# Kernel optimization log

Hardware: AMD Instinct MI355X
Metric: run time of the kernel (lower is better)

The kernel has to match this reference:

```python
import jax, jax.numpy as jnp
import numpy as np

B, S, D, H = 32, 8192, 128, 128


def setup_inputs() -> dict:
    key = jax.random.key(0)
    ks = jax.random.split(key, 8)
    x = jax.random.normal(ks[0], (B, D), dtype=jnp.float32)
    context = jax.random.normal(ks[1], (B, S, D), dtype=jnp.float32)
    mask = jax.random.bernoulli(ks[2], 0.3, (B, S))
    mask = mask.at[:, 0].set(False)
    W_in = jax.random.normal(ks[3], (H, D), dtype=jnp.float32) / np.sqrt(D)
    b_in = jax.random.normal(ks[4], (H,), dtype=jnp.float32) * 0.01
    # torch Conv1d(D, H, 1) weight is [H, D, 1]; squeeze kernel dim -> [H, D]
    W_ctx = jax.random.normal(ks[5], (H, D), dtype=jnp.float32) / np.sqrt(D)
    b_ctx = jax.random.normal(ks[6], (H,), dtype=jnp.float32) * 0.01
    V = jax.random.uniform(ks[7], (H,), dtype=jnp.float32, minval=-1.0, maxval=1.0)
    return {"x": x, "context": context, "mask": mask, "W_in": W_in,
            "b_in": b_in, "W_ctx": W_ctx, "b_ctx": b_ctx, "V": V}


def reference(x, context, mask, W_in, b_in, W_ctx, b_ctx, V):
    # x: [B, D] decoder hidden state; context: [B, S, D]; mask: [B, S] bool (True = masked)
    inp = x @ W_in.T + b_in                                  # [B, H]
    # Conv1d with kernel size 1 == pointwise linear over D
    ctx = jnp.einsum('bsd,hd->bhs', context, W_ctx) + b_ctx[None, :, None]  # [B, H, S]
    att = jnp.einsum('h,bhs->bs', V, jnp.tanh(inp[:, :, None] + ctx))       # [B, S]
    att = jnp.where(mask, -jnp.inf, att)
    alpha = jax.nn.softmax(att, axis=1)                      # [B, S]
    hidden_state = jnp.einsum('bhs,bs->bh', ctx, alpha)      # [B, H]
    return hidden_state, att
```

## Files before the change

### kernel.cpp

```cpp
#include <hip/hip_runtime.h>
#include <math.h>

#define BB 32
#define SS 8192
#define DD 128
#define HH 128

#define MASK_NEG (-1e30f)

#define WSHIFT 32.0f

typedef _Float16 half8 __attribute__((ext_vector_type(8)));
typedef float f32x4 __attribute__((ext_vector_type(4)));

__device__ __forceinline__ float fast_tanh(float x) {
    float t = __expf(2.0f * x);
    return 1.0f - 2.0f / (t + 1.0f);
}

__global__ __launch_bounds__(128) void k_inp(const float* __restrict__ x,
                                             const float* __restrict__ W_in,
                                             const float* __restrict__ b_in,
                                             const float* __restrict__ b_ctx,
                                             float* __restrict__ inp2) {
    int b = blockIdx.x;
    int h = threadIdx.x;
    const float* xr = x + b * DD;
    const float* wr = W_in + h * DD;
    float a0 = 0.f, a1 = 0.f, a2 = 0.f, a3 = 0.f;
#pragma unroll
    for (int d = 0; d < DD; d += 4) {
        a0 = fmaf(xr[d + 0], wr[d + 0], a0);
        a1 = fmaf(xr[d + 1], wr[d + 1], a1);
        a2 = fmaf(xr[d + 2], wr[d + 2], a2);
        a3 = fmaf(xr[d + 3], wr[d + 3], a3);
    }
    inp2[b * HH + h] = b_in[h] + b_ctx[h] + ((a0 + a1) + (a2 + a3));
}

__global__ __launch_bounds__(256) void k_wswz(const float* __restrict__ W_ctx,
                                              _Float16* __restrict__ Whs,
                                              _Float16* __restrict__ Wls) {
    int i = blockIdx.x * 256 + threadIdx.x;
    int fi = i >> 9;
    int lane = (i >> 3) & 63;
    int j = i & 7;
    int mt = fi >> 2, ksi = fi & 3;
    int row = mt * 16 + (lane & 15);
    int k = ksi * 32 + (lane >> 4) * 8 + j;
    float w = W_ctx[row * DD + k];
    _Float16 hi = (_Float16)w;
    Whs[i] = hi;
    Wls[i] = (_Float16)(w - (float)hi);
}

__device__ __forceinline__ void split8(const float4 a, const float4 b, half8& hi,
                                       half8& lo) {
    float f0 = a.x, f1 = a.y, f2 = a.z, f3 = a.w;
    float f4 = b.x, f5 = b.y, f6 = b.z, f7 = b.w;
    hi[0] = (_Float16)f0; lo[0] = (_Float16)(f0 - (float)hi[0]);
    hi[1] = (_Float16)f1; lo[1] = (_Float16)(f1 - (float)hi[1]);
    hi[2] = (_Float16)f2; lo[2] = (_Float16)(f2 - (float)hi[2]);
    hi[3] = (_Float16)f3; lo[3] = (_Float16)(f3 - (float)hi[3]);
    hi[4] = (_Float16)f4; lo[4] = (_Float16)(f4 - (float)hi[4]);
    hi[5] = (_Float16)f5; lo[5] = (_Float16)(f5 - (float)hi[5]);
    hi[6] = (_Float16)f6; lo[6] = (_Float16)(f6 - (float)hi[6]);
    hi[7] = (_Float16)f7; lo[7] = (_Float16)(f7 - (float)hi[7]);
}

__global__ __launch_bounds__(512, 2) void k_att(const float* __restrict__ context,
                                                const unsigned char* __restrict__ mask,
                                                const _Float16* __restrict__ Whs,
                                                const _Float16* __restrict__ Wls,
                                                const float* __restrict__ V,
                                                const float* __restrict__ inp2,
                                                float* __restrict__ att_out,
                                                float* __restrict__ cbarU,
                                                float* __restrict__ Lsum) {
    const int b = blockIdx.y;
    const int sg = blockIdx.x;
    const int tid = threadIdx.x;

    __shared__ __align__(16) unsigned char smem[68608];
    __shared__ float redL[8];
    _Float16* WhsL = (_Float16*)smem;
    _Float16* WlsL = (_Float16*)(smem + 32768);
    float* vib = (float*)(smem + 65536);
    float* warr = (float*)(smem + 66560);
    float* CP = (float*)smem;

    {
        const float4* gh = (const float4*)Whs;
        const float4* gl = (const float4*)Wls;
        float4* lh = (float4*)WhsL;
        float4* ll = (float4*)WlsL;
#pragma unroll
        for (int i = 0; i < 4; ++i) {
            lh[i * 512 + tid] = gh[i * 512 + tid];
            ll[i * 512 + tid] = gl[i * 512 + tid];
        }
    }
    if (tid < HH) {
        ((float2*)vib)[tid] = make_float2(inp2[b * HH + tid], V[tid]);
    }

    const int wv = tid >> 6;
    const int lane = tid & 63;
    const int ln = lane & 15;
    const int quad = lane >> 4;
    const int s_base = sg * 512 + wv * 16 + ln;

    const float* crow = context + ((size_t)b * SS + s_base) * DD + quad * 8;

    float wsum = 0.f;

    __syncthreads();

#pragma unroll 1
    for (int t = 0; t < 4; ++t) {
        const float* trow = crow + (size_t)t * 128 * DD;
        float4 cf[8];
#pragma unroll
        for (int ks = 0; ks < 4; ++ks) {
            cf[2 * ks + 0] = *(const float4*)(trow + ks * 32);
            cf[2 * ks + 1] = *(const float4*)(trow + ks * 32 + 4);
        }

        half8 bH[4], bL[4];
#pragma unroll
        for (int ksi = 0; ksi < 4; ++ksi)
            split8(cf[2 * ksi + 0], cf[2 * ksi + 1], bH[ksi], bL[ksi]);

        float p = 0.f;
#pragma unroll
        for (int mt = 0; mt < 8; ++mt) {
            f32x4 acc = (f32x4){0.f, 0.f, 0.f, 0.f};
#pragma unroll
            for (int ksi = 0; ksi < 4; ++ksi) {
                const int off = (mt * 4 + ksi) * 512 + lane * 8;
                half8 aH = *(const half8*)&WhsL[off];
                half8 aL = *(const half8*)&WlsL[off];
                acc = __builtin_amdgcn_mfma_f32_16x16x32_f16(aH, bH[ksi], acc, 0, 0, 0);
                acc = __builtin_amdgcn_mfma_f32_16x16x32_f16(aL, bH[ksi], acc, 0, 0, 0);
                acc = __builtin_amdgcn_mfma_f32_16x16x32_f16(aH, bL[ksi], acc, 0, 0, 0);
            }
            const f32x4 va = *(const f32x4*)(vib + mt * 32 + quad * 8);
            const f32x4 vc = *(const f32x4*)(vib + mt * 32 + quad * 8 + 4);
            p = fmaf(va[1], fast_tanh(acc[0] + va[0]), p);
            p = fmaf(va[3], fast_tanh(acc[1] + va[2]), p);
            p = fmaf(vc[1], fast_tanh(acc[2] + vc[0]), p);
            p = fmaf(vc[3], fast_tanh(acc[3] + vc[2]), p);
        }
        p += __shfl_xor(p, 16);
        p += __shfl_xor(p, 32);

        const int s = s_base + t * 128;
        const size_t idx = (size_t)b * SS + s;
        const bool msk = mask[idx];
        const float w = msk ? 0.f : __expf(p - WSHIFT);
        wsum += w;

        if (quad == 0) {
            att_out[idx] = msk ? MASK_NEG : p;
            warr[t * 128 + wv * 16 + ln] = w;
        }
    }

#pragma unroll
    for (int off = 1; off < 64; off <<= 1) wsum += __shfl_xor(wsum, off);
    if (lane == 0) redL[wv] = wsum * 0.25f;

    __syncthreads();

    {
        const int d = tid & 127;
        const int chunk = tid >> 7;
        const float* cbase =
            context + ((size_t)b * SS + sg * 512 + chunk * 128) * DD + d;
        const float* wrow = warr + chunk * 128;
        float acc = 0.f;
#pragma unroll 8
        for (int r = 0; r < 128; ++r)
            acc = fmaf(wrow[r], cbase[(size_t)r * DD], acc);
        CP[chunk * 128 + d] = acc;
    }
    __syncthreads();

    if (tid < DD) {
        float ssum = CP[tid] + CP[128 + tid] + CP[256 + tid] + CP[384 + tid];
        atomicAdd(&cbarU[b * DD + tid], ssum);
    }
    if (tid == 0) {
        float ls = 0.f;
#pragma unroll
        for (int i = 0; i < 8; ++i) ls += redL[i];
        atomicAdd(&Lsum[b], ls);
    }
}

__global__ __launch_bounds__(256) void k_hidden(const float* __restrict__ cbarU,
                                                const float* __restrict__ Lsum,
                                                const float* __restrict__ W_ctx,
                                                const float* __restrict__ b_ctx,
                                                float* __restrict__ hidden) {
    const int idx = blockIdx.x * 256 + threadIdx.x;
    const int b = idx >> 7;
    const int h = idx & 127;
    const float invL = 1.0f / Lsum[b];
    const float* cb = cbarU + b * DD;
    const float* w = W_ctx + h * DD;
    float a0 = 0.f, a1 = 0.f, a2 = 0.f, a3 = 0.f;
#pragma unroll
    for (int d = 0; d < DD; d += 4) {
        a0 = fmaf(cb[d + 0], w[d + 0], a0);
        a1 = fmaf(cb[d + 1], w[d + 1], a1);
        a2 = fmaf(cb[d + 2], w[d + 2], a2);
        a3 = fmaf(cb[d + 3], w[d + 3], a3);
    }
    hidden[b * HH + h] = b_ctx[h] + ((a0 + a1) + (a2 + a3)) * invL;
}

extern "C" void kernel_launch(void* const* d_in, const int* in_sizes, int n_in,
                              void* d_out, int out_size, void* d_ws, size_t ws_size,
                              hipStream_t stream) {
    const float* x = (const float*)d_in[0];
    const float* context = (const float*)d_in[1];
    const unsigned char* mask = (const unsigned char*)d_in[2];
    const float* W_in = (const float*)d_in[3];
    const float* b_in = (const float*)d_in[4];
    const float* W_ctx = (const float*)d_in[5];
    const float* b_ctx = (const float*)d_in[6];
    const float* V = (const float*)d_in[7];

    float* out = (float*)d_out;
    float* hidden = out;
    float* att = out + BB * HH;

    float* ws = (float*)d_ws;
    float* inp2 = ws;
    float* cbarU = inp2 + BB * HH;
    float* Lsum = cbarU + BB * DD;
    _Float16* Whs = (_Float16*)(Lsum + BB);
    _Float16* Wls = Whs + HH * DD;

    hipMemsetAsync(cbarU, 0, (BB * DD + BB) * sizeof(float), stream);

    k_wswz<<<dim3(DD * HH / 256), dim3(256), 0, stream>>>(W_ctx, Whs, Wls);
    k_inp<<<dim3(BB), dim3(HH), 0, stream>>>(x, W_in, b_in, b_ctx, inp2);
    k_att<<<dim3(SS / 512, BB), dim3(512), 0, stream>>>(context, mask, Whs, Wls, V,
                                                        inp2, att, cbarU, Lsum);
    k_hidden<<<dim3(BB * HH / 256), dim3(256), 0, stream>>>(cbarU, Lsum, W_ctx, b_ctx,
                                                            hidden);
}
```

Baseline: 237.3 us.

## Fuse weight swizzle and input projection into attention kernel, drop atomics and memset

Removes the separate W_ctx swizzle kernel, the input projection kernel and the memset. Each attention block now splits and swizzles W_ctx into LDS and computes its own input projection. The atomics are replaced by per-segment partial buffers that k_hidden reduces. The context tile for the next iteration is also prefetched into registers while the current one is processed. This cuts launch and serialization overhead, at the cost of redundant per-block weight conversion and projection work and higher register pressure.

```diff
diff --git a/kernel.cpp b/kernel.cpp
--- a/kernel.cpp
+++ b/kernel.cpp
@@ -16,42 +16,6 @@
 __device__ __forceinline__ float fast_tanh(float x) {
     float t = __expf(2.0f * x);
     return 1.0f - 2.0f / (t + 1.0f);
-}
-
-__global__ __launch_bounds__(128) void k_inp(const float* __restrict__ x,
-                                             const float* __restrict__ W_in,
-                                             const float* __restrict__ b_in,
-                                             const float* __restrict__ b_ctx,
-                                             float* __restrict__ inp2) {
-    int b = blockIdx.x;
-    int h = threadIdx.x;
-    const float* xr = x + b * DD;
-    const float* wr = W_in + h * DD;
-    float a0 = 0.f, a1 = 0.f, a2 = 0.f, a3 = 0.f;
-#pragma unroll
-    for (int d = 0; d < DD; d += 4) {
-        a0 = fmaf(xr[d + 0], wr[d + 0], a0);
-        a1 = fmaf(xr[d + 1], wr[d + 1], a1);
-        a2 = fmaf(xr[d + 2], wr[d + 2], a2);
-        a3 = fmaf(xr[d + 3], wr[d + 3], a3);
-    }
-    inp2[b * HH + h] = b_in[h] + b_ctx[h] + ((a0 + a1) + (a2 + a3));
-}
-
-__global__ __launch_bounds__(256) void k_wswz(const float* __restrict__ W_ctx,
-                                              _Float16* __restrict__ Whs,
-                                              _Float16* __restrict__ Wls) {
-    int i = blockIdx.x * 256 + threadIdx.x;
-    int fi = i >> 9;
-    int lane = (i >> 3) & 63;
-    int j = i & 7;
-    int mt = fi >> 2, ksi = fi & 3;
-    int row = mt * 16 + (lane & 15);
-    int k = ksi * 32 + (lane >> 4) * 8 + j;
-    float w = W_ctx[row * DD + k];
-    _Float16 hi = (_Float16)w;
-    Whs[i] = hi;
-    Wls[i] = (_Float16)(w - (float)hi);
 }
 
 __device__ __forceinline__ void split8(const float4 a, const float4 b, half8& hi,
@@ -68,15 +32,17 @@
     hi[7] = (_Float16)f7; lo[7] = (_Float16)(f7 - (float)hi[7]);
 }
 
-__global__ __launch_bounds__(512, 2) void k_att(const float* __restrict__ context,
+__global__ __launch_bounds__(512, 2) void k_att(const float* __restrict__ x,
+                                                const float* __restrict__ context,
                                                 const unsigned char* __restrict__ mask,
-                                                const _Float16* __restrict__ Whs,
-                                                const _Float16* __restrict__ Wls,
+                                                const float* __restrict__ W_in,
+                                                const float* __restrict__ b_in,
+                                                const float* __restrict__ W_ctx,
+                                                const float* __restrict__ b_ctx,
                                                 const float* __restrict__ V,
-                                                const float* __restrict__ inp2,
                                                 float* __restrict__ att_out,
-                                                float* __restrict__ cbarU,
-                                                float* __restrict__ Lsum) {
+                                                float* __restrict__ cbarP,
+                                                float* __restrict__ LsumP) {
     const int b = blockIdx.y;
     const int sg = blockIdx.x;
     const int tid = threadIdx.x;
@@ -89,21 +55,6 @@
     float* warr = (float*)(smem + 66560);
     float* CP = (float*)smem;
 
-    {
-        const float4* gh = (const float4*)Whs;
-        const float4* gl = (const float4*)Wls;
-        float4* lh = (float4*)WhsL;
-        float4* ll = (float4*)WlsL;
-#pragma unroll
-        for (int i = 0; i < 4; ++i) {
-            lh[i * 512 + tid] = gh[i * 512 + tid];
-            ll[i * 512 + tid] = gl[i * 512 + tid];
-        }
-    }
-    if (tid < HH) {
-        ((float2*)vib)[tid] = make_float2(inp2[b * HH + tid], V[tid]);
-    }
-
     const int wv = tid >> 6;
     const int lane = tid & 63;
     const int ln = lane & 15;
@@ -112,24 +63,68 @@
 
     const float* crow = context + ((size_t)b * SS + s_base) * DD + quad * 8;
 
+    float4 cfA[8];
+#pragma unroll
+    for (int ks = 0; ks < 4; ++ks) {
+        cfA[2 * ks + 0] = *(const float4*)(crow + ks * 32);
+        cfA[2 * ks + 1] = *(const float4*)(crow + ks * 32 + 4);
+    }
+
+#pragma unroll
+    for (int i = 0; i < 4; ++i) {
+        const int c = i * 512 + tid;
+        const int row = c >> 4;
+        const int kb = c & 15;
+        const float4 wa = ((const float4*)W_ctx)[2 * c];
+        const float4 wb = ((const float4*)W_ctx)[2 * c + 1];
+        half8 hi, lo;
+        split8(wa, wb, hi, lo);
+        const int dst =
+            ((row >> 4) * 4 + (kb >> 2)) * 512 + ((row & 15) + ((kb & 3) << 4)) * 8;
+        *(half8*)&WhsL[dst] = hi;
+        *(half8*)&WlsL[dst] = lo;
+    }
+
+    {
+        const int h = tid & 127;
+        const int part = tid >> 7;
+        const float* xr = x + b * DD + part * 32;
+        const float* wr = W_in + h * DD + part * 32;
+        float a0 = 0.f, a1 = 0.f, a2 = 0.f, a3 = 0.f;
+#pragma unroll
+        for (int d = 0; d < 32; d += 4) {
+            a0 = fmaf(xr[d + 0], wr[d + 0], a0);
+            a1 = fmaf(xr[d + 1], wr[d + 1], a1);
+            a2 = fmaf(xr[d + 2], wr[d + 2], a2);
+            a3 = fmaf(xr[d + 3], wr[d + 3], a3);
+        }
+        warr[tid] = (a0 + a1) + (a2 + a3);
+    }
+    __syncthreads();
+    if (tid < HH) {
+        const float ib = warr[tid] + warr[128 + tid] + warr[256 + tid] +
+                         warr[384 + tid] + b_in[tid] + b_ctx[tid];
+        ((float2*)vib)[tid] = make_float2(ib, V[tid]);
+    }
+    __syncthreads();
+
     float wsum = 0.f;
-
-    __syncthreads();
 
 #pragma unroll 1
     for (int t = 0; t < 4; ++t) {
-        const float* trow = crow + (size_t)t * 128 * DD;
-        float4 cf[8];
-#pragma unroll
-        for (int ks = 0; ks < 4; ++ks) {
-            cf[2 * ks + 0] = *(const float4*)(trow + ks * 32);
-            cf[2 * ks + 1] = *(const float4*)(trow + ks * 32 + 4);
-        }
-
         half8 bH[4], bL[4];
 #pragma unroll
         for (int ksi = 0; ksi < 4; ++ksi)
-            split8(cf[2 * ksi + 0], cf[2 * ksi + 1], bH[ksi], bL[ksi]);
+            split8(cfA[2 * ksi + 0], cfA[2 * ksi + 1], bH[ksi], bL[ksi]);
+
+        if (t < 3) {
+            const float* nrow = crow + (size_t)(t + 1) * 128 * DD;
+#pragma unroll
+            for (int ks = 0; ks < 4; ++ks) {
+                cfA[2 * ks + 0] = *(const float4*)(nrow + ks * 32);
+                cfA[2 * ks + 1] = *(const float4*)(nrow + ks * 32 + 4);
+            }
+        }
 
         float p = 0.f;
 #pragma unroll
@@ -187,27 +182,40 @@
     __syncthreads();
 
     if (tid < DD) {
-        float ssum = CP[tid] + CP[128 + tid] + CP[256 + tid] + CP[384 + tid];
-        atomicAdd(&cbarU[b * DD + tid], ssum);
+        const float ssum = CP[tid] + CP[128 + tid] + CP[256 + tid] + CP[384 + tid];
+        cbarP[((size_t)sg * BB + b) * DD + tid] = ssum;
     }
     if (tid == 0) {
         float ls = 0.f;
 #pragma unroll
         for (int i = 0; i < 8; ++i) ls += redL[i];
-        atomicAdd(&Lsum[b], ls);
-    }
-}
-
-__global__ __launch_bounds__(256) void k_hidden(const float* __restrict__ cbarU,
-                                                const float* __restrict__ Lsum,
+        LsumP[sg * BB + b] = ls;
+    }
+}
+
+__global__ __launch_bounds__(128) void k_hidden(const float* __restrict__ cbarP,
+                                                const float* __restrict__ LsumP,
                                                 const float* __restrict__ W_ctx,
                                                 const float* __restrict__ b_ctx,
                                                 float* __restrict__ hidden) {
-    const int idx = blockIdx.x * 256 + threadIdx.x;
-    const int b = idx >> 7;
-    const int h = idx & 127;
-    const float invL = 1.0f / Lsum[b];
-    const float* cb = cbarU + b * DD;
+    const int b = blockIdx.x;
+    const int h = threadIdx.x;
+    __shared__ float cb[DD];
+    __shared__ float Lsh;
+    {
+        float s = 0.f;
+#pragma unroll
+        for (int sg = 0; sg < 16; ++sg) s += cbarP[((size_t)sg * BB + b) * DD + h];
+        cb[h] = s;
+    }
+    if (h == 0) {
+        float l = 0.f;
+#pragma unroll
+        for (int sg = 0; sg < 16; ++sg) l += LsumP[sg * BB + b];
+        Lsh = l;
+    }
+    __syncthreads();
+    const float invL = 1.0f / Lsh;
     const float* w = W_ctx + h * DD;
     float a0 = 0.f, a1 = 0.f, a2 = 0.f, a3 = 0.f;
 #pragma unroll
@@ -237,18 +245,10 @@
     float* att = out + BB * HH;
 
     float* ws = (float*)d_ws;
-    float* inp2 = ws;
-    float* cbarU = inp2 + BB * HH;
-    float* Lsum = cbarU + BB * DD;
-    _Float16* Whs = (_Float16*)(Lsum + BB);
-    _Float16* Wls = Whs + HH * DD;
-
-    hipMemsetAsync(cbarU, 0, (BB * DD + BB) * sizeof(float), stream);
-
-    k_wswz<<<dim3(DD * HH / 256), dim3(256), 0, stream>>>(W_ctx, Whs, Wls);
-    k_inp<<<dim3(BB), dim3(HH), 0, stream>>>(x, W_in, b_in, b_ctx, inp2);
-    k_att<<<dim3(SS / 512, BB), dim3(512), 0, stream>>>(context, mask, Whs, Wls, V,
-                                                        inp2, att, cbarU, Lsum);
-    k_hidden<<<dim3(BB * HH / 256), dim3(256), 0, stream>>>(cbarU, Lsum, W_ctx, b_ctx,
-                                                            hidden);
-}
+    float* cbarP = ws;
+    float* LsumP = cbarP + 16 * BB * DD;
+
+    k_att<<<dim3(SS / 512, BB), dim3(512), 0, stream>>>(
+        x, context, mask, W_in, b_in, W_ctx, b_ctx, V, att, cbarP, LsumP);
+    k_hidden<<<dim3(BB), dim3(HH), 0, stream>>>(cbarP, LsumP, W_ctx, b_ctx, hidden);
+}
```

Measured after the change: 225.4 us. 1.05x faster.
